# Optimization experiments

Measured on AMD Instinct MI355X. Metric: run time of the kernel, lower is better.

Reference implementation:

```python
import jax, jax.numpy as jnp
import numpy as np
from jax import lax

EPS = 1e-4  # BatchNorm eps from the module
K = 3       # kernel_size
PAD = 1     # padding


def setup_inputs() -> dict:
    key = jax.random.key(0)
    k1, k2, k3 = jax.random.split(key, 3)
    N, Cin, H, Wd = 32, 256, 56, 56
    Cout = 256
    x = jax.random.normal(k1, (N, Cin, H, Wd), dtype=jnp.float32)
    gamma = jnp.ones((Cin,), dtype=jnp.float32)
    beta_bn = jnp.zeros((Cin,), dtype=jnp.float32)
    W = jax.random.normal(k2, (Cout, Cin, K, K), dtype=jnp.float32) * 0.05
    b = jax.random.normal(k3, (Cout,), dtype=jnp.float32) * 0.01
    return {"x": x, "gamma": gamma, "beta_bn": beta_bn, "W": W, "b": b}


def _conv(x, w, padding):
    return lax.conv_general_dilated(
        x, w, window_strides=(1, 1),
        padding=[(padding, padding), (padding, padding)],
        dimension_numbers=("NCHW", "OIHW", "NCHW"))


def reference(x, gamma, beta_bn, W, b):
    # BatchNorm2d in training mode: batch statistics over (N, H, W), biased var
    mu = jnp.mean(x, axis=(0, 2, 3), keepdims=True)
    var = jnp.var(x, axis=(0, 2, 3), keepdims=True)
    xn = (x - mu) * lax.rsqrt(var + EPS)
    xn = xn * gamma[None, :, None, None] + beta_bn[None, :, None, None]

    # BinActiv: per-pixel channel-mean of |x|, then sign-binarize
    m = jnp.mean(jnp.abs(xn), axis=1, keepdims=True)  # [N,1,H,W]
    xb = jnp.sign(xn)

    # Binarize weights; alpha = L1 norm per output filter / n
    n = W.shape[1] * W.shape[2] * W.shape[3]
    alpha = jnp.sum(jnp.abs(W), axis=(1, 2, 3)) / n  # [Cout]
    Wb = jnp.sign(W)

    y = _conv(xb, Wb, PAD) + b[None, :, None, None]

    # beta map: box filter (stride 1) over channel-mean magnitudes
    box = jnp.full((1, 1, K, K), 1.0 / (K * K), dtype=x.dtype)
    beta_map = _conv(m, box, PAD)  # [N,1,Ho,Wo]

    out = jax.nn.relu(y * beta_map * alpha[None, :, None, None])
    return out
```

## Files before the change

kernel.cpp:

```cpp
#include <hip/hip_runtime.h>
#include <cstdint>
#include <cstddef>

#define N_    32
#define C_    256
#define H_    56
#define W_    56
#define HW_   (H_ * W_)
#define NHW_  (N_ * HW_)
#define COUT_ 256
#define EPS_  1e-4f
#define PW_   58
#define PIMG_ (PW_ * PW_)

__global__ void k_bn_partial(const float* __restrict__ x,
                             float* __restrict__ ps, float* __restrict__ pq) {
    const int c = blockIdx.x >> 3;
    const int s = blockIdx.x & 7;
    const int t = threadIdx.x;
    float sm = 0.f, sq = 0.f;
    for (int n = s * 4; n < s * 4 + 4; ++n) {
        const float4* p = (const float4*)(x + (size_t)(n * C_ + c) * HW_);
        for (int i = t; i < HW_ / 4; i += 256) {
            float4 v = p[i];
            sm += v.x + v.y + v.z + v.w;
            sq += v.x * v.x + v.y * v.y + v.z * v.z + v.w * v.w;
        }
    }
    __shared__ float ls[256], lq[256];
    ls[t] = sm; lq[t] = sq;
    __syncthreads();
    for (int off = 128; off >= 1; off >>= 1) {
        if (t < off) { ls[t] += ls[t + off]; lq[t] += lq[t + off]; }
        __syncthreads();
    }
    if (t == 0) { ps[s * C_ + c] = ls[0]; pq[s * C_ + c] = lq[0]; }
}

__global__ void k_bn_final(const float* __restrict__ ps, const float* __restrict__ pq,
                           const float* __restrict__ gamma, const float* __restrict__ beta,
                           float* __restrict__ a, float* __restrict__ bb) {
    const int c = threadIdx.x;
    float sm = 0.f, sq = 0.f;
    for (int s = 0; s < 8; ++s) { sm += ps[s * C_ + c]; sq += pq[s * C_ + c]; }
    float mu   = sm * (1.f / NHW_);
    float var  = sq * (1.f / NHW_) - mu * mu;
    float rstd = rsqrtf(var + EPS_);
    float g    = gamma[c] * rstd;
    a[c]  = g;
    bb[c] = beta[c] - mu * g;
}

__global__ void k_wpack(const float* __restrict__ Wt, float* __restrict__ alpha,
                        uint64_t* __restrict__ wbits, int* __restrict__ ctab) {
    const int co = blockIdx.x;
    const int ci = threadIdx.x;
    const int lane = ci & 63, wave = ci >> 6;
    const float* p = Wt + (size_t)(co * C_ + ci) * 9;
    float wv[9];
    float asum = 0.f;
#pragma unroll
    for (int t = 0; t < 9; ++t) { wv[t] = p[t]; asum += fabsf(wv[t]); }
    __shared__ int Pl[9];
    if (ci < 9) Pl[ci] = 0;
    __syncthreads();
#pragma unroll
    for (int t = 0; t < 9; ++t) {
        uint64_t mask = __ballot(wv[t] > 0.f);
        if (lane == 0) {
            wbits[(co * 9 + t) * 4 + wave] = mask;
            atomicAdd(&Pl[t], (int)__popcll(mask));
        }
    }
    __shared__ float red[256];
    red[ci] = asum;
    __syncthreads();
    for (int off = 128; off >= 1; off >>= 1) {
        if (ci < off) red[ci] += red[ci + off];
        __syncthreads();
    }
    if (ci == 0) alpha[co] = red[0] * (1.f / 2304.f);
    if (ci < 9) {
        const int rc = ci / 3, cc = ci % 3;
        unsigned m9 = (rc == 0 ? 0x007u : 0u) | (rc == 2 ? 0x1C0u : 0u)
                    | (cc == 0 ? 0x049u : 0u) | (cc == 2 ? 0x124u : 0u);
        int s = 0;
#pragma unroll
        for (int t = 0; t < 9; ++t)
            if ((m9 >> t) & 1) s += 2 * Pl[t] - 256;
        ctab[ci * 256 + co] = s;
    }
}

__global__ void k_mpack(const float* __restrict__ x, const float* __restrict__ a,
                        const float* __restrict__ bb, uint64_t* __restrict__ xbits,
                        float* __restrict__ m) {
    const int p = blockIdx.x * 256 + threadIdx.x;
    const int n = p / HW_;
    const int hw = p - n * HW_;
    const int h = hw / W_;
    const int w = hw - h * W_;
    const float* xp = x + (size_t)n * C_ * HW_ + hw;
    float macc = 0.f;
    uint64_t bits[4];
#pragma unroll
    for (int wd = 0; wd < 4; ++wd) {
        uint64_t bw = 0;
#pragma unroll
        for (int j = 0; j < 64; ++j) {
            const int c = wd * 64 + j;
            float xn = fmaf(xp[(size_t)c * HW_], a[c], bb[c]);
            macc += fabsf(xn);
            bw |= (xn > 0.f) ? (1ull << j) : 0ull;
        }
        bits[wd] = bw;
    }
    ulonglong2* xb = (ulonglong2*)(xbits + ((size_t)n * PIMG_ + (size_t)(h + 1) * PW_ + (w + 1)) * 4);
    xb[0] = make_ulonglong2(bits[0], bits[1]);
    xb[1] = make_ulonglong2(bits[2], bits[3]);
    m[p] = macc * (1.f / C_);
}

__global__ void k_box(const float* __restrict__ m, float* __restrict__ beta_map) {
    const int idx = blockIdx.x * 256 + threadIdx.x;
    if (idx >= NHW_) return;
    const int w = idx % W_;
    const int h = (idx / W_) % H_;
    const int n = idx / HW_;
    const float* mp = m + (size_t)n * HW_;
    float s = 0.f;
#pragma unroll
    for (int dh = 0; dh < 3; ++dh) {
        int ih = h + dh - 1;
        if (ih < 0 || ih >= H_) continue;
#pragma unroll
        for (int dw = 0; dw < 3; ++dw) {
            int iw = w + dw - 1;
            if (iw < 0 || iw >= W_) continue;
            s += mp[ih * W_ + iw];
        }
    }
    beta_map[idx] = s * (1.f / 9.f);
}

__global__ void __launch_bounds__(256, 4)
k_conv(const uint64_t* __restrict__ xbits, const uint64_t* __restrict__ wbits,
       const int* __restrict__ ctab, const float* __restrict__ beta_map,
       const float* __restrict__ alpha, const float* __restrict__ bias,
       float* __restrict__ out) {
    const int p   = blockIdx.x * 256 + (int)threadIdx.x;
    const int grp = blockIdx.y;
    const int n  = p / HW_;
    const int hw = p - n * HW_;
    const int h  = hw / W_;
    const int w  = hw - h * W_;

    const uint64_t* xb = xbits + ((size_t)n * PIMG_ + (size_t)h * PW_ + w) * 4;
    uint64_t xw[36];
#pragma unroll
    for (int dh = 0; dh < 3; ++dh)
#pragma unroll
        for (int dw = 0; dw < 3; ++dw) {
            const uint64_t* tp = xb + ((size_t)dh * PW_ + dw) * 4;
#pragma unroll
            for (int wd = 0; wd < 4; ++wd)
                xw[(dh * 3 + dw) * 4 + wd] = tp[wd];
        }

    const int rowcls = (h == 0) ? 0 : ((h == H_ - 1) ? 2 : 1);
    const int colcls = (w == 0) ? 0 : ((w == W_ - 1) ? 2 : 1);
    const int* crow = ctab + (rowcls * 3 + colcls) * 256 + grp * 64;

    const float bm = beta_map[p];
    float* op = out + (size_t)n * COUT_ * HW_ + (size_t)(grp * 64) * HW_ + hw;

    for (int coi = 0; coi < 64; ++coi) {
        const int co = grp * 64 + coi;
        const uint64_t* wq = wbits + (size_t)co * 36;
        int a0 = 0, a1 = 0, a2 = 0, a3 = 0;
#pragma unroll
        for (int t = 0; t < 9; ++t) {
            a0 += __popcll(xw[t * 4 + 0] ^ wq[t * 4 + 0]);
            a1 += __popcll(xw[t * 4 + 1] ^ wq[t * 4 + 1]);
            a2 += __popcll(xw[t * 4 + 2] ^ wq[t * 4 + 2]);
            a3 += __popcll(xw[t * 4 + 3] ^ wq[t * 4 + 3]);
        }
        const int acc = (a0 + a1) + (a2 + a3);
        const int dot = 2304 - 2 * acc + crow[coi];
        float o = ((float)dot + bias[co]) * bm * alpha[co];
        o = fmaxf(o, 0.f);
        op[(size_t)coi * HW_] = o;
    }
}

extern "C" void kernel_launch(void* const* d_in, const int* in_sizes, int n_in,
                              void* d_out, int out_size, void* d_ws, size_t ws_size,
                              hipStream_t stream) {
    (void)in_sizes; (void)n_in; (void)out_size; (void)ws_size;
    const float* x     = (const float*)d_in[0];
    const float* gamma = (const float*)d_in[1];
    const float* betab = (const float*)d_in[2];
    const float* Wt    = (const float*)d_in[3];
    const float* b     = (const float*)d_in[4];
    float* out = (float*)d_out;

    uint8_t* base = (uint8_t*)d_ws;
    float*    ps       = (float*)(base + 0);
    float*    pq       = (float*)(base + 8192);
    float*    a        = (float*)(base + 16384);
    float*    bb       = (float*)(base + 17408);
    float*    alpha    = (float*)(base + 18432);
    int*      ctab     = (int*)(base + 19456);
    uint64_t* wbits    = (uint64_t*)(base + 28672);
    uint64_t* xbits    = (uint64_t*)(base + 102400);
    float*    m        = (float*)(base + 3547136);
    float*    beta_map = (float*)(base + 3948544);

    k_bn_partial<<<2048, 256, 0, stream>>>(x, ps, pq);
    k_bn_final<<<1, 256, 0, stream>>>(ps, pq, gamma, betab, a, bb);
    k_wpack<<<COUT_, 256, 0, stream>>>(Wt, alpha, wbits, ctab);
    hipMemsetAsync(xbits, 0, (size_t)N_ * PIMG_ * 4 * sizeof(uint64_t), stream);
    k_mpack<<<NHW_ / 256, 256, 0, stream>>>(x, a, bb, xbits, m);
    k_box<<<(NHW_ + 255) / 256, 256, 0, stream>>>(m, beta_map);
    k_conv<<<dim3(NHW_ / 256, 4), 256, 0, stream>>>(xbits, wbits, ctab, beta_map, alpha, b, out);
}
```

Measured before the change: 338.3 us.

## Split mpack across channel words and stage conv weight bits in LDS

k_mpack now launches four times as many blocks, each handling one 64-channel word, which raises parallelism for the memory-bound binarize pass. The per-pixel channel mean is accumulated with atomicAdd into m, so m is zeroed with an added memset. k_conv copies its group's 64x36 weight words into shared memory once per block instead of reading them from global memory for each output channel, and loads the activation bits as 128-bit vectors. The costs are float atomics, whose summation order is nondeterministic, an extra memset, and 18KB of LDS per block, which can limit occupancy.

```diff
diff --git a/kernel.cpp b/kernel.cpp
--- a/kernel.cpp
+++ b/kernel.cpp
@@ -96,29 +96,23 @@
                         const float* __restrict__ bb, uint64_t* __restrict__ xbits,
                         float* __restrict__ m) {
     const int p = blockIdx.x * 256 + threadIdx.x;
+    const int wd = blockIdx.y;
     const int n = p / HW_;
     const int hw = p - n * HW_;
     const int h = hw / W_;
     const int w = hw - h * W_;
-    const float* xp = x + (size_t)n * C_ * HW_ + hw;
+    const float* xp = x + (size_t)n * C_ * HW_ + (size_t)(wd * 64) * HW_ + hw;
     float macc = 0.f;
-    uint64_t bits[4];
-#pragma unroll
-    for (int wd = 0; wd < 4; ++wd) {
-        uint64_t bw = 0;
-#pragma unroll
-        for (int j = 0; j < 64; ++j) {
-            const int c = wd * 64 + j;
-            float xn = fmaf(xp[(size_t)c * HW_], a[c], bb[c]);
-            macc += fabsf(xn);
-            bw |= (xn > 0.f) ? (1ull << j) : 0ull;
-        }
-        bits[wd] = bw;
-    }
-    ulonglong2* xb = (ulonglong2*)(xbits + ((size_t)n * PIMG_ + (size_t)(h + 1) * PW_ + (w + 1)) * 4);
-    xb[0] = make_ulonglong2(bits[0], bits[1]);
-    xb[1] = make_ulonglong2(bits[2], bits[3]);
-    m[p] = macc * (1.f / C_);
+    uint64_t bw = 0;
+#pragma unroll
+    for (int j = 0; j < 64; ++j) {
+        const int c = wd * 64 + j;
+        float xn = fmaf(xp[(size_t)j * HW_], a[c], bb[c]);
+        macc += fabsf(xn);
+        bw |= (xn > 0.f) ? (1ull << j) : 0ull;
+    }
+    xbits[((size_t)n * PIMG_ + (size_t)(h + 1) * PW_ + (w + 1)) * 4 + wd] = bw;
+    atomicAdd(&m[p], macc * (1.f / C_));
 }
 
 __global__ void k_box(const float* __restrict__ m, float* __restrict__ beta_map) {
@@ -155,16 +149,25 @@
     const int h  = hw / W_;
     const int w  = hw - h * W_;
 
+    __shared__ uint64_t wsm[64 * 36];
+    {
+        const uint64_t* gw = wbits + (size_t)grp * (64 * 36);
+        for (int k = threadIdx.x; k < 64 * 36; k += 256) wsm[k] = gw[k];
+    }
+
     const uint64_t* xb = xbits + ((size_t)n * PIMG_ + (size_t)h * PW_ + w) * 4;
     uint64_t xw[36];
 #pragma unroll
     for (int dh = 0; dh < 3; ++dh)
 #pragma unroll
         for (int dw = 0; dw < 3; ++dw) {
-            const uint64_t* tp = xb + ((size_t)dh * PW_ + dw) * 4;
-#pragma unroll
-            for (int wd = 0; wd < 4; ++wd)
-                xw[(dh * 3 + dw) * 4 + wd] = tp[wd];
+            const ulonglong2* tp = (const ulonglong2*)(xb + ((size_t)dh * PW_ + dw) * 4);
+            ulonglong2 v0 = tp[0];
+            ulonglong2 v1 = tp[1];
+            xw[(dh * 3 + dw) * 4 + 0] = v0.x;
+            xw[(dh * 3 + dw) * 4 + 1] = v0.y;
+            xw[(dh * 3 + dw) * 4 + 2] = v1.x;
+            xw[(dh * 3 + dw) * 4 + 3] = v1.y;
         }
 
     const int rowcls = (h == 0) ? 0 : ((h == H_ - 1) ? 2 : 1);
@@ -174,16 +177,18 @@
     const float bm = beta_map[p];
     float* op = out + (size_t)n * COUT_ * HW_ + (size_t)(grp * 64) * HW_ + hw;
 
+    __syncthreads();
+
     for (int coi = 0; coi < 64; ++coi) {
         const int co = grp * 64 + coi;
-        const uint64_t* wq = wbits + (size_t)co * 36;
+        const uint64_t* wq = wsm + coi * 36;
         int a0 = 0, a1 = 0, a2 = 0, a3 = 0;
 #pragma unroll
         for (int t = 0; t < 9; ++t) {
-            a0 += __popcll(xw[t * 4 + 0] ^ wq[t * 4 + 0]);
-            a1 += __popcll(xw[t * 4 + 1] ^ wq[t * 4 + 1]);
-            a2 += __popcll(xw[t * 4 + 2] ^ wq[t * 4 + 2]);
-            a3 += __popcll(xw[t * 4 + 3] ^ wq[t * 4 + 3]);
+            a0 += (int)__popcll(xw[t * 4 + 0] ^ wq[t * 4 + 0]);
+            a1 += (int)__popcll(xw[t * 4 + 1] ^ wq[t * 4 + 1]);
+            a2 += (int)__popcll(xw[t * 4 + 2] ^ wq[t * 4 + 2]);
+            a3 += (int)__popcll(xw[t * 4 + 3] ^ wq[t * 4 + 3]);
         }
         const int acc = (a0 + a1) + (a2 + a3);
         const int dot = 2304 - 2 * acc + crow[coi];
@@ -220,7 +225,8 @@
     k_bn_final<<<1, 256, 0, stream>>>(ps, pq, gamma, betab, a, bb);
     k_wpack<<<COUT_, 256, 0, stream>>>(Wt, alpha, wbits, ctab);
     hipMemsetAsync(xbits, 0, (size_t)N_ * PIMG_ * 4 * sizeof(uint64_t), stream);
-    k_mpack<<<NHW_ / 256, 256, 0, stream>>>(x, a, bb, xbits, m);
+    hipMemsetAsync(m, 0, (size_t)NHW_ * sizeof(float), stream);
+    k_mpack<<<dim3(NHW_ / 256, 4), 256, 0, stream>>>(x, a, bb, xbits, m);
     k_box<<<(NHW_ + 255) / 256, 256, 0, stream>>>(m, beta_map);
     k_conv<<<dim3(NHW_ / 256, 4), 256, 0, stream>>>(xbits, wbits, ctab, beta_map, alpha, b, out);
 }
```

New measurement: 352.3 us. 1.04x slower.
